# Performance work log

Hardware: AMD Instinct MI355X
Metric: run time of the kernel (lower is better)

Reference implementation:

```python
import jax, jax.numpy as jnp
import numpy as np
from math import sqrt

B, H, S, D = 4, 16, 2048, 64
NEG = -1000000000.0

def setup_inputs() -> dict:
    key = jax.random.key(0)
    kq, kk, kv, km = jax.random.split(key, 4)
    Q = jax.random.normal(kq, (B, H, S, D), dtype=jnp.float32)
    K = jax.random.normal(kk, (B, H, S, D), dtype=jnp.float32)
    V = jax.random.normal(kv, (B, H, S, D), dtype=jnp.float32)
    mask = jax.random.uniform(km, (B, 1, S, S)) < 0.1
    return {"Q": Q, "K": K, "V": V, "mask": mask}

def reference(Q, K, V, mask) -> jnp.ndarray:
    # scores: [B,H,S,S]
    scores = jnp.einsum('bhqd,bhkd->bhqk', Q, K)
    scores = jnp.where(mask, NEG, scores)
    attn = jax.nn.softmax(scores / sqrt(Q.shape[-1]), axis=-1)
    return jnp.einsum('bhqk,bhkd->bhqd', attn, V)
```

## Files before the change

### kernel.cpp

```cpp
#include <hip/hip_runtime.h>
#include <hip/hip_bf16.h>


#define SEQ 2048
#define DIM 64
#define NBH 64
#define LOG2E 1.44269504088896340736f
#define SCL (0.125f * LOG2E)
#define NEG_SCALED -1.25e8f

typedef short bf16x8 __attribute__((ext_vector_type(8)));
typedef float f32x4 __attribute__((ext_vector_type(4)));
typedef float f32x16 __attribute__((ext_vector_type(16)));

static __device__ __forceinline__ unsigned short f2bf(float f) {
    unsigned int u = __float_as_uint(f);
    u += 0x7fffu + ((u >> 16) & 1u);
    return (unsigned short)(u >> 16);
}

static __device__ __forceinline__ unsigned int pkbf(float a, float b) {
    __hip_bfloat162 t = __float22bfloat162_rn(make_float2(a, b));
    union { __hip_bfloat162 h; unsigned int u; } c; c.h = t;
    return c.u;
}

#define GLD16(gp, lp) __builtin_amdgcn_global_load_lds( \
    (const __attribute__((address_space(1))) unsigned int*)(gp), \
    (__attribute__((address_space(3))) unsigned int*)(lp), 16, 0, 0)

__global__ __launch_bounds__(256)
void prep_all_kernel(const float* __restrict__ K, const float* __restrict__ V,
                     const int* __restrict__ M,
                     unsigned short* __restrict__ Kb, unsigned short* __restrict__ Vt,
                     unsigned int* __restrict__ Mpt) {
    const int x  = blockIdx.x;
    const int r7 = x % 7;
    const int g  = x / 7;
    const int t  = threadIdx.x;
    if (r7 < 4) {
        const int idx = g * 4 + r7;
        size_t i0 = ((size_t)idx * 256 + t) * 8;
        float4 a = *(const float4*)(K + i0);
        float4 b = *(const float4*)(K + i0 + 4);
        union { uint4 u; unsigned short s[8]; } w;
        w.s[0] = f2bf(a.x); w.s[1] = f2bf(a.y); w.s[2] = f2bf(a.z); w.s[3] = f2bf(a.w);
        w.s[4] = f2bf(b.x); w.s[5] = f2bf(b.y); w.s[6] = f2bf(b.z); w.s[7] = f2bf(b.w);
        *(uint4*)(Kb + i0) = w.u;
    } else if (r7 < 6) {
        __shared__ __align__(16) unsigned short T[64 * 64];
        const int vb = g * 2 + (r7 - 4);
        const int bh = vb >> 5;
        const int k0 = (vb & 31) * 64;
        {
            const int kk = t >> 2;
            const int c  = t & 3;
            const int u  = (kk & ~12) | ((kk & 4) << 1) | ((kk & 8) >> 1);
            const int cs = c ^ ((u >> 3) & 3);
            const float* vp = V + ((size_t)bh * SEQ + k0 + kk) * DIM + c * 16;
            union { uint4 q[2]; unsigned short s[16]; } w;
            #pragma unroll
            for (int j = 0; j < 16; ++j) w.s[j] = f2bf(vp[j]);
            *(uint4*)&T[u * 64 + cs * 16]     = w.q[0];
            *(uint4*)&T[u * 64 + cs * 16 + 8] = w.q[1];
        }
        __syncthreads();
        {
            const int kc = t & 7;
            const int dp = t >> 3;
            const int ch = (dp >> 3) ^ (kc & 3);
            const unsigned int* T32 = (const unsigned int*)T;
            union { uint4 u; unsigned short s[8]; } o0, o1;
            #pragma unroll
            for (int i = 0; i < 8; ++i) {
                unsigned int v = T32[(8 * kc + i) * 32 + ch * 8 + (dp & 7)];
                o0.s[i] = (unsigned short)v;
                o1.s[i] = (unsigned short)(v >> 16);
            }
            unsigned short* op = Vt + ((size_t)bh * DIM + 2 * dp) * SEQ + k0 + 8 * kc;
            *(uint4*)op         = o0.u;
            *(uint4*)(op + SEQ) = o1.u;
        }
    } else {
        __shared__ unsigned int Wt[64][8];
        const int b  = g >> 8;
        const int q0 = ((g >> 3) & 31) * 64;
        const int k0 = (g & 7) * 256;
        const int w  = t >> 6, l = t & 63;
        #pragma unroll 4
        for (int row = 0; row < 16; ++row) {
            const int q = q0 + w * 16 + row;
            int4 v4 = *(const int4*)(M + ((size_t)b * SEQ + q) * SEQ + k0 + l * 4);
            unsigned int nib = (unsigned int)(v4.x != 0) | ((unsigned int)(v4.y != 0) << 1)
                             | ((unsigned int)(v4.z != 0) << 2) | ((unsigned int)(v4.w != 0) << 3);
            unsigned int v = nib << (4 * (l & 7));
            v |= __shfl_xor(v, 1);
            v |= __shfl_xor(v, 2);
            v |= __shfl_xor(v, 4);
            if ((l & 7) == 0) Wt[w * 16 + row][l >> 3] = v;
        }
        __syncthreads();
        {
            const int q = t & 63, g0 = t >> 6;
            #pragma unroll
            for (int gg = 0; gg < 2; ++gg) {
                const int gi = g0 + gg * 4;
                Mpt[((size_t)b * 64 + (k0 >> 5) + gi) * SEQ + q0 + q] = Wt[q][gi];
            }
        }
    }
}

__global__ __launch_bounds__(256, 4)
void attn_main_kernel(const float* __restrict__ Q,
                      const unsigned short* __restrict__ Kb,
                      const unsigned short* __restrict__ Vt,
                      const unsigned int* __restrict__ Mpt,
                      float* __restrict__ O)
{
    const int bh   = blockIdx.y;
    const int b    = bh >> 4;
    const int q0   = blockIdx.x * 128;
    const int tid  = threadIdx.x;
    const int wave = tid >> 6;
    const int lane = tid & 63;
    const int h    = lane >> 5;
    const int q32  = lane & 31;

    __shared__ __align__(16) unsigned short Kt[2][4096];
    __shared__ __align__(16) unsigned short Vs[2][4096];

    const unsigned short* Kbh = Kb + (size_t)bh * SEQ * DIM;
    const unsigned short* Vbh = Vt + (size_t)bh * SEQ * DIM;

    bf16x8 qf[4];
    {
        const float* qp = Q + ((size_t)bh * SEQ + q0 + wave * 32 + q32) * DIM + h * 8;
        #pragma unroll
        for (int dc = 0; dc < 4; ++dc) {
            float4 xx = *(const float4*)(qp + dc * 16);
            float4 yy = *(const float4*)(qp + dc * 16 + 4);
            qf[dc][0] = (short)f2bf(xx.x * SCL); qf[dc][1] = (short)f2bf(xx.y * SCL);
            qf[dc][2] = (short)f2bf(xx.z * SCL); qf[dc][3] = (short)f2bf(xx.w * SCL);
            qf[dc][4] = (short)f2bf(yy.x * SCL); qf[dc][5] = (short)f2bf(yy.y * SCL);
            qf[dc][6] = (short)f2bf(yy.z * SCL); qf[dc][7] = (short)f2bf(yy.w * SCL);
        }
    }

    const int kkey  = wave * 8 + (lane >> 3);
    const int kclog = (lane & 7) ^ (lane >> 3);
    const unsigned short* kp = Kbh + (size_t)kkey * DIM + kclog * 8;
    const int vd    = wave * 16 + (lane >> 2);
    const int vclog = (lane & 3) ^ ((lane >> 3) & 3);
    const unsigned short* vp = Vbh + (size_t)vd * SEQ + vclog * 8;

    int kofs[4], vofs[4];
    #pragma unroll
    for (int dc = 0; dc < 4; ++dc)
        kofs[dc] = q32 * 64 + (((dc * 2 + h) ^ (q32 & 7)) * 8);
    #pragma unroll
    for (int kk = 0; kk < 2; ++kk)
        #pragma unroll
        for (int dh = 0; dh < 2; ++dh)
            vofs[kk * 2 + dh] = (dh * 32 + q32) * 32 + (((kk * 2 + h) ^ ((q32 >> 1) & 3)) * 8);

    const unsigned int* mpc = Mpt + (size_t)b * 64 * SEQ + (q0 + wave * 32 + q32);

    f32x16 acc[2];
    #pragma unroll
    for (int i = 0; i < 16; ++i) { acc[0][i] = 0.f; acc[1][i] = 0.f; }
    float lsum = 0.f;

    {
        unsigned short* kd = &Kt[0][wave * 512];
        unsigned short* vdst = &Vs[0][wave * 512];
        GLD16(kp, kd);
        GLD16(kp + 2048, kd + 2048);
        GLD16(vp, vdst);
        GLD16(vp + 32, vdst + 2048);
    }

    for (int it = 0; it < SEQ / 64; ++it) {
        __syncthreads();

        unsigned int mw0 = mpc[0];
        unsigned int mw1 = mpc[SEQ];
        mpc += 2 * SEQ;

        if (it + 1 < SEQ / 64) {
            const unsigned short* kn = kp + (size_t)(it + 1) * 64 * DIM;
            const unsigned short* vn = vp + (size_t)(it + 1) * 64;
            const int nb = (it + 1) & 1;
            unsigned short* kd = &Kt[nb][wave * 512];
            unsigned short* vdst = &Vs[nb][wave * 512];
            GLD16(kn, kd);
            GLD16(kn + 2048, kd + 2048);
            GLD16(vn, vdst);
            GLD16(vn + 32, vdst + 2048);
        }

        const unsigned short* Ktb = Kt[it & 1];
        const unsigned short* Vsb = Vs[it & 1];

        f32x16 sc0, sc1;
        #pragma unroll
        for (int i = 0; i < 16; ++i) { sc0[i] = 0.f; sc1[i] = 0.f; }
        #pragma unroll
        for (int dc = 0; dc < 4; ++dc) {
            bf16x8 kf0 = *(const bf16x8*)(Ktb + kofs[dc]);
            sc0 = __builtin_amdgcn_mfma_f32_32x32x16_bf16(kf0, qf[dc], sc0, 0, 0, 0);
        }
        #pragma unroll
        for (int dc = 0; dc < 4; ++dc) {
            bf16x8 kf1 = *(const bf16x8*)(Ktb + 2048 + kofs[dc]);
            sc1 = __builtin_amdgcn_mfma_f32_32x32x16_bf16(kf1, qf[dc], sc1, 0, 0, 0);
        }

        unsigned int pk0[8];
        {
            const unsigned int mq = mw0 >> (4 * h);
            float pv[16];
            #pragma unroll
            for (int r = 0; r < 16; ++r) {
                const int s = (r & 3) + 8 * (r >> 2);
                float e = __builtin_amdgcn_exp2f(sc0[r]);
                pv[r] = ((mq >> s) & 1u) ? 0.f : e;
                lsum += pv[r];
            }
            #pragma unroll
            for (int m = 0; m < 8; ++m) pk0[m] = pkbf(pv[2 * m], pv[2 * m + 1]);
        }

        #pragma unroll
        for (int kk = 0; kk < 2; ++kk) {
            union { unsigned int u[4]; bf16x8 v; } fr;
            fr.u[0] = pk0[4 * kk + 0]; fr.u[1] = pk0[4 * kk + 1];
            fr.u[2] = pk0[4 * kk + 2]; fr.u[3] = pk0[4 * kk + 3];
            #pragma unroll
            for (int dh = 0; dh < 2; ++dh) {
                bf16x8 vf = *(const bf16x8*)(Vsb + vofs[kk * 2 + dh]);
                acc[dh] = __builtin_amdgcn_mfma_f32_32x32x16_bf16(vf, fr.v, acc[dh], 0, 0, 0);
            }
        }

        unsigned int pk1[8];
        {
            const unsigned int mq = mw1 >> (4 * h);
            float pv[16];
            #pragma unroll
            for (int r = 0; r < 16; ++r) {
                const int s = (r & 3) + 8 * (r >> 2);
                float e = __builtin_amdgcn_exp2f(sc1[r]);
                pv[r] = ((mq >> s) & 1u) ? 0.f : e;
                lsum += pv[r];
            }
            #pragma unroll
            for (int m = 0; m < 8; ++m) pk1[m] = pkbf(pv[2 * m], pv[2 * m + 1]);
        }

        #pragma unroll
        for (int kk = 0; kk < 2; ++kk) {
            union { unsigned int u[4]; bf16x8 v; } fr;
            fr.u[0] = pk1[4 * kk + 0]; fr.u[1] = pk1[4 * kk + 1];
            fr.u[2] = pk1[4 * kk + 2]; fr.u[3] = pk1[4 * kk + 3];
            #pragma unroll
            for (int dh = 0; dh < 2; ++dh) {
                bf16x8 vf = *(const bf16x8*)(Vsb + 2048 + vofs[kk * 2 + dh]);
                acc[dh] = __builtin_amdgcn_mfma_f32_32x32x16_bf16(vf, fr.v, acc[dh], 0, 0, 0);
            }
        }
    }

    lsum += __shfl_xor(lsum, 32);
    const float inv = 1.f / lsum;
    float* orow = O + ((size_t)bh * SEQ + q0 + wave * 32 + q32) * DIM;
    #pragma unroll
    for (int dh = 0; dh < 2; ++dh) {
        #pragma unroll
        for (int r23 = 0; r23 < 4; ++r23) {
            float4 w;
            w.x = acc[dh][4 * r23 + 0] * inv;
            w.y = acc[dh][4 * r23 + 1] * inv;
            w.z = acc[dh][4 * r23 + 2] * inv;
            w.w = acc[dh][4 * r23 + 3] * inv;
            *(float4*)(orow + dh * 32 + r23 * 8 + h * 4) = w;
        }
    }
}

__global__ __launch_bounds__(256)
void attn_fallback_kernel(const float* __restrict__ Q,
                          const float* __restrict__ K,
                          const float* __restrict__ V,
                          const int* __restrict__ mask,
                          float* __restrict__ O)
{
    const int bh   = blockIdx.y;
    const int b    = bh >> 4;
    const int q0   = blockIdx.x * 64;
    const int tid  = threadIdx.x;
    const int wave = tid >> 6;
    const int lane = tid & 63;
    const int quad = lane >> 4;
    const int l16  = lane & 15;

    __shared__ __align__(16) unsigned short Klds[32][72];
    __shared__ __align__(16) unsigned short VT[64][40];
    __shared__ __align__(16) unsigned short Plds[4][16][40];

    const float* Qb = Q + (size_t)bh * SEQ * DIM;
    const float* Kbp = K + (size_t)bh * SEQ * DIM;
    const float* Vb = V + (size_t)bh * SEQ * DIM;
    const int*   Mb = mask + (size_t)b * SEQ * SEQ;

    const int qrow_frag = q0 + wave * 16 + l16;
    bf16x8 qf0, qf1;
    {
        const float* qp = Qb + (size_t)qrow_frag * DIM + quad * 8;
        #pragma unroll
        for (int i = 0; i < 8; ++i) {
            qf0[i] = (short)f2bf(qp[i]);
            qf1[i] = (short)f2bf(qp[32 + i]);
        }
    }

    f32x4 acc[4];
    #pragma unroll
    for (int dg = 0; dg < 4; ++dg) acc[dg] = (f32x4){0.f, 0.f, 0.f, 0.f};
    float mrowv[4] = {-INFINITY, -INFINITY, -INFINITY, -INFINITY};
    float lrow[4] = {0.f, 0.f, 0.f, 0.f};

    const int skey = tid >> 3;
    const int sd0  = (tid & 7) * 8;
    const int vkey = tid & 31;
    const int vd0  = (tid >> 5) * 8;
    const int qrow_m = q0 + wave * 16 + quad * 4;

    for (int kb = 0; kb < SEQ; kb += 32) {
        __syncthreads();
        {
            const float* kpp = Kbp + (size_t)(kb + skey) * DIM + sd0;
            union { uint4 u4; unsigned short s[8]; } kw;
            #pragma unroll
            for (int i = 0; i < 8; ++i) kw.s[i] = f2bf(kpp[i]);
            *(uint4*)&Klds[skey][sd0] = kw.u4;
        }
        {
            const float* vpp = Vb + (size_t)(kb + vkey) * DIM + vd0;
            #pragma unroll
            for (int i = 0; i < 8; ++i) VT[vd0 + i][vkey] = f2bf(vpp[i]);
        }
        __syncthreads();

        f32x4 scr[2];
        scr[0] = (f32x4){0.f, 0.f, 0.f, 0.f};
        scr[1] = (f32x4){0.f, 0.f, 0.f, 0.f};
        #pragma unroll
        for (int nt = 0; nt < 2; ++nt) {
            bf16x8 kf0 = *(const bf16x8*)&Klds[nt * 16 + l16][quad * 8];
            bf16x8 kf1 = *(const bf16x8*)&Klds[nt * 16 + l16][32 + quad * 8];
            scr[nt] = __builtin_amdgcn_mfma_f32_16x16x32_bf16(qf0, kf0, scr[nt], 0, 0, 0);
            scr[nt] = __builtin_amdgcn_mfma_f32_16x16x32_bf16(qf1, kf1, scr[nt], 0, 0, 0);
        }

        float x[2][4];
        #pragma unroll
        for (int nt = 0; nt < 2; ++nt)
            #pragma unroll
            for (int r = 0; r < 4; ++r) {
                int mv = Mb[(size_t)(qrow_m + r) * SEQ + kb + nt * 16 + l16];
                x[nt][r] = mv ? NEG_SCALED : scr[nt][r] * 0.125f;
            }

        float p[2][4];
        #pragma unroll
        for (int r = 0; r < 4; ++r) {
            float rm = fmaxf(x[0][r], x[1][r]);
            #pragma unroll
            for (int off = 1; off < 16; off <<= 1)
                rm = fmaxf(rm, __shfl_xor(rm, off, 16));
            float mn = fmaxf(mrowv[r], rm);
            float alpha = exp2f((mrowv[r] - mn) * LOG2E);
            mrowv[r] = mn;
            float p0 = exp2f((x[0][r] - mn) * LOG2E);
            float p1 = exp2f((x[1][r] - mn) * LOG2E);
            p[0][r] = p0; p[1][r] = p1;
            float rs = p0 + p1;
            #pragma unroll
            for (int off = 1; off < 16; off <<= 1)
                rs += __shfl_xor(rs, off, 16);
            lrow[r] = lrow[r] * alpha + rs;
            #pragma unroll
            for (int dg = 0; dg < 4; ++dg)
                acc[dg][r] *= alpha;
        }

        #pragma unroll
        for (int nt = 0; nt < 2; ++nt)
            #pragma unroll
            for (int r = 0; r < 4; ++r)
                Plds[wave][quad * 4 + r][nt * 16 + l16] = f2bf(p[nt][r]);

        bf16x8 pf = *(const bf16x8*)&Plds[wave][l16][quad * 8];

        #pragma unroll
        for (int dg = 0; dg < 4; ++dg) {
            bf16x8 vf = *(const bf16x8*)&VT[dg * 16 + l16][quad * 8];
            acc[dg] = __builtin_amdgcn_mfma_f32_16x16x32_bf16(pf, vf, acc[dg], 0, 0, 0);
        }
    }

    float* Ob = O + (size_t)bh * SEQ * DIM;
    #pragma unroll
    for (int r = 0; r < 4; ++r) {
        float inv = 1.f / lrow[r];
        #pragma unroll
        for (int dg = 0; dg < 4; ++dg)
            Ob[(size_t)(qrow_m + r) * DIM + dg * 16 + l16] = acc[dg][r] * inv;
    }
}

extern "C" void kernel_launch(void* const* d_in, const int* in_sizes, int n_in,
                              void* d_out, int out_size, void* d_ws, size_t ws_size,
                              hipStream_t stream) {
    const float* Q = (const float*)d_in[0];
    const float* K = (const float*)d_in[1];
    const float* V = (const float*)d_in[2];
    const int* mask = (const int*)d_in[3];
    float*        O = (float*)d_out;

    const size_t szK = (size_t)NBH * SEQ * DIM * 2;
    const size_t szV = (size_t)NBH * SEQ * DIM * 2;
    const size_t szM = (size_t)4 * SEQ * (SEQ / 32) * 4;
    const size_t need = szK + szV + szM;

    if (ws_size >= need) {
        unsigned short* KbW = (unsigned short*)d_ws;
        unsigned short* VtW = (unsigned short*)((char*)d_ws + szK);
        unsigned int*  MptW = (unsigned int*)((char*)d_ws + szK + szV);

        prep_all_kernel<<<dim3(7168), 256, 0, stream>>>(K, V, mask, KbW, VtW, MptW);
        attn_main_kernel<<<dim3(SEQ / 128, NBH), 256, 0, stream>>>(Q, KbW, VtW, MptW, O);
    } else {
        attn_fallback_kernel<<<dim3(SEQ / 64, NBH), 256, 0, stream>>>(Q, K, V, mask, O);
    }
}
```

Baseline: 288.7 us.

## Restructure prep kernel blocks and batch loads; seed MFMA chain from zero

The prep kernel's interleaved modulo-7 block mapping becomes contiguous block ranges. K conversion now processes four chunks per block, which shrinks the grid. Loads are vectorised and issued in batches: V rows use float4 reads with packed bf16 conversion, and mask rows are all loaded before being processed, to raise memory-level parallelism. The main kernel's first MFMA now takes a zero constant instead of an explicit zeroing loop, which trims per-iteration instructions. The costs are higher register use in the prep kernel and a small change in how bf16 rounding is done (pkbf instead of the manual f2bf).

```diff
diff --git a/kernel.cpp b/kernel.cpp
--- a/kernel.cpp
+++ b/kernel.cpp
@@ -34,22 +34,28 @@
                      const int* __restrict__ M,
                      unsigned short* __restrict__ Kb, unsigned short* __restrict__ Vt,
                      unsigned int* __restrict__ Mpt) {
-    const int x  = blockIdx.x;
-    const int r7 = x % 7;
-    const int g  = x / 7;
-    const int t  = threadIdx.x;
-    if (r7 < 4) {
-        const int idx = g * 4 + r7;
-        size_t i0 = ((size_t)idx * 256 + t) * 8;
-        float4 a = *(const float4*)(K + i0);
-        float4 b = *(const float4*)(K + i0 + 4);
-        union { uint4 u; unsigned short s[8]; } w;
-        w.s[0] = f2bf(a.x); w.s[1] = f2bf(a.y); w.s[2] = f2bf(a.z); w.s[3] = f2bf(a.w);
-        w.s[4] = f2bf(b.x); w.s[5] = f2bf(b.y); w.s[6] = f2bf(b.z); w.s[7] = f2bf(b.w);
-        *(uint4*)(Kb + i0) = w.u;
-    } else if (r7 < 6) {
+    const int x = blockIdx.x;
+    const int t = threadIdx.x;
+    if (x < 1024) {
+        const size_t base = (size_t)x * 8192 + t * 8;
+        float4 f[4][2];
+        #pragma unroll
+        for (int s = 0; s < 4; ++s) {
+            f[s][0] = *(const float4*)(K + base + s * 2048);
+            f[s][1] = *(const float4*)(K + base + s * 2048 + 4);
+        }
+        #pragma unroll
+        for (int s = 0; s < 4; ++s) {
+            uint4 w;
+            w.x = pkbf(f[s][0].x, f[s][0].y);
+            w.y = pkbf(f[s][0].z, f[s][0].w);
+            w.z = pkbf(f[s][1].x, f[s][1].y);
+            w.w = pkbf(f[s][1].z, f[s][1].w);
+            *(uint4*)(Kb + base + s * 2048) = w;
+        }
+    } else if (x < 3072) {
         __shared__ __align__(16) unsigned short T[64 * 64];
-        const int vb = g * 2 + (r7 - 4);
+        const int vb = x - 1024;
         const int bh = vb >> 5;
         const int k0 = (vb & 31) * 64;
         {
@@ -58,11 +64,16 @@
             const int u  = (kk & ~12) | ((kk & 4) << 1) | ((kk & 8) >> 1);
             const int cs = c ^ ((u >> 3) & 3);
             const float* vp = V + ((size_t)bh * SEQ + k0 + kk) * DIM + c * 16;
-            union { uint4 q[2]; unsigned short s[16]; } w;
-            #pragma unroll
-            for (int j = 0; j < 16; ++j) w.s[j] = f2bf(vp[j]);
-            *(uint4*)&T[u * 64 + cs * 16]     = w.q[0];
-            *(uint4*)&T[u * 64 + cs * 16 + 8] = w.q[1];
+            float4 g[4];
+            #pragma unroll
+            for (int j = 0; j < 4; ++j) g[j] = *(const float4*)(vp + j * 4);
+            uint4 w0, w1;
+            w0.x = pkbf(g[0].x, g[0].y); w0.y = pkbf(g[0].z, g[0].w);
+            w0.z = pkbf(g[1].x, g[1].y); w0.w = pkbf(g[1].z, g[1].w);
+            w1.x = pkbf(g[2].x, g[2].y); w1.y = pkbf(g[2].z, g[2].w);
+            w1.z = pkbf(g[3].x, g[3].y); w1.w = pkbf(g[3].z, g[3].w);
+            *(uint4*)&T[u * 64 + cs * 16]     = w0;
+            *(uint4*)&T[u * 64 + cs * 16 + 8] = w1;
         }
         __syncthreads();
         {
@@ -83,14 +94,20 @@
         }
     } else {
         __shared__ unsigned int Wt[64][8];
+        const int g  = x - 3072;
         const int b  = g >> 8;
         const int q0 = ((g >> 3) & 31) * 64;
         const int k0 = (g & 7) * 256;
         const int w  = t >> 6, l = t & 63;
-        #pragma unroll 4
+        int4 vals[16];
+        #pragma unroll
         for (int row = 0; row < 16; ++row) {
             const int q = q0 + w * 16 + row;
-            int4 v4 = *(const int4*)(M + ((size_t)b * SEQ + q) * SEQ + k0 + l * 4);
+            vals[row] = *(const int4*)(M + ((size_t)b * SEQ + q) * SEQ + k0 + l * 4);
+        }
+        #pragma unroll
+        for (int row = 0; row < 16; ++row) {
+            int4 v4 = vals[row];
             unsigned int nib = (unsigned int)(v4.x != 0) | ((unsigned int)(v4.y != 0) << 1)
                              | ((unsigned int)(v4.z != 0) << 2) | ((unsigned int)(v4.w != 0) << 3);
             unsigned int v = nib << (4 * (l & 7));
@@ -171,6 +188,10 @@
     for (int i = 0; i < 16; ++i) { acc[0][i] = 0.f; acc[1][i] = 0.f; }
     float lsum = 0.f;
 
+    f32x16 zc;
+    #pragma unroll
+    for (int i = 0; i < 16; ++i) zc[i] = 0.f;
+
     {
         unsigned short* kd = &Kt[0][wave * 512];
         unsigned short* vdst = &Vs[0][wave * 512];
@@ -203,17 +224,23 @@
         const unsigned short* Vsb = Vs[it & 1];
 
         f32x16 sc0, sc1;
-        #pragma unroll
-        for (int i = 0; i < 16; ++i) { sc0[i] = 0.f; sc1[i] = 0.f; }
-        #pragma unroll
-        for (int dc = 0; dc < 4; ++dc) {
-            bf16x8 kf0 = *(const bf16x8*)(Ktb + kofs[dc]);
-            sc0 = __builtin_amdgcn_mfma_f32_32x32x16_bf16(kf0, qf[dc], sc0, 0, 0, 0);
-        }
-        #pragma unroll
-        for (int dc = 0; dc < 4; ++dc) {
-            bf16x8 kf1 = *(const bf16x8*)(Ktb + 2048 + kofs[dc]);
-            sc1 = __builtin_amdgcn_mfma_f32_32x32x16_bf16(kf1, qf[dc], sc1, 0, 0, 0);
+        {
+            bf16x8 kf = *(const bf16x8*)(Ktb + kofs[0]);
+            sc0 = __builtin_amdgcn_mfma_f32_32x32x16_bf16(kf, qf[0], zc, 0, 0, 0);
+        }
+        #pragma unroll
+        for (int dc = 1; dc < 4; ++dc) {
+            bf16x8 kf = *(const bf16x8*)(Ktb + kofs[dc]);
+            sc0 = __builtin_amdgcn_mfma_f32_32x32x16_bf16(kf, qf[dc], sc0, 0, 0, 0);
+        }
+        {
+            bf16x8 kf = *(const bf16x8*)(Ktb + 2048 + kofs[0]);
+            sc1 = __builtin_amdgcn_mfma_f32_32x32x16_bf16(kf, qf[0], zc, 0, 0, 0);
+        }
+        #pragma unroll
+        for (int dc = 1; dc < 4; ++dc) {
+            bf16x8 kf = *(const bf16x8*)(Ktb + 2048 + kofs[dc]);
+            sc1 = __builtin_amdgcn_mfma_f32_32x32x16_bf16(kf, qf[dc], sc1, 0, 0, 0);
         }
 
         unsigned int pk0[8];
@@ -439,7 +466,7 @@
         unsigned short* VtW = (unsigned short*)((char*)d_ws + szK);
         unsigned int*  MptW = (unsigned int*)((char*)d_ws + szK + szV);
 
-        prep_all_kernel<<<dim3(7168), 256, 0, stream>>>(K, V, mask, KbW, VtW, MptW);
+        prep_all_kernel<<<dim3(4096), 256, 0, stream>>>(K, V, mask, KbW, VtW, MptW);
         attn_main_kernel<<<dim3(SEQ / 128, NBH), 256, 0, stream>>>(Q, KbW, VtW, MptW, O);
     } else {
         attn_fallback_kernel<<<dim3(SEQ / 64, NBH), 256, 0, stream>>>(Q, K, V, mask, O);
```

Measured after the change: 278.9 us. -3.4%, faster.
